# Kernel optimization log

Measured on AMD Instinct MI355X. Metric: run time of the kernel, lower is better.

## Reference

```python
import jax, jax.numpy as jnp
import numpy as np

B, T, D_IN, H, C = 4096, 20, 300, 512, 10


def setup_inputs() -> dict:
    key = jax.random.key(0)
    ks = jax.random.split(key, 12)
    s = lambda fan_in, fan_out: float(np.sqrt(6.0 / (fan_in + fan_out)))  # xavier uniform bound
    u = lambda k, shape, b: jax.random.uniform(k, shape, jnp.float32, -b, b)
    return {
        "x": jax.random.normal(ks[0], (B, T, D_IN), jnp.float32),
        "W_emb": u(ks[1], (D_IN, H), s(D_IN, H)),
        "b_emb": jnp.zeros((H,), jnp.float32),
        "wx0": u(ks[2], (H, H), s(H, H)),
        "wh0": u(ks[3], (H, H), s(H, H)),
        "b0": jnp.zeros((H,), jnp.float32),
        "wx1": u(ks[4], (H, H), s(H, H)),
        "wh1": u(ks[5], (H, H), s(H, H)),
        "b1": jnp.zeros((H,), jnp.float32),
        "wx2": u(ks[6], (H, H), s(H, H)),
        "wh2": u(ks[7], (H, H), s(H, H)),
        "b2": jnp.zeros((H,), jnp.float32),
        "W_fc": u(ks[8], (H, C), s(H, C)),
        "b_fc": jnp.zeros((C,), jnp.float32),
    }


def reference(x, W_emb, b_emb, wx0, wh0, b0, wx1, wh1, b1, wx2, wh2, b2, W_fc, b_fc):
    # embedding_layer applied to all timesteps: [B,T,300] -> [B,T,512]
    emb = jnp.einsum("btd,dh->bth", x, W_emb) + b_emb
    h0 = jnp.zeros((x.shape[0], wx0.shape[1]), x.dtype)
    init = (h0, h0, h0)

    def step(carry, v_t):  # v_t: [B,H]
        h0, h1, h2 = carry
        h0 = jnp.tanh(v_t @ wx0 + h0 @ wh0 + b0)
        h1 = jnp.tanh(h0 @ wx1 + h1 @ wh1 + b1)
        h2 = jnp.tanh(h1 @ wx2 + h2 @ wh2 + b2)
        return (h0, h1, h2), None

    (h0, h1, h2), _ = jax.lax.scan(step, init, jnp.swapaxes(emb, 0, 1))  # scan over T
    return h2 @ W_fc + b_fc  # [B, C]
```

## Files before the change

### kernel.cpp

```cpp
#include <hip/hip_runtime.h>

typedef _Float16 f16;
typedef _Float16 f16x8 __attribute__((ext_vector_type(8)));
typedef float floatx4 __attribute__((ext_vector_type(4)));

__device__ __forceinline__ float ftanh(float x) {
  float ax = __builtin_fabsf(x);
  float e  = __expf(-2.0f * ax);
  float t  = (1.0f - e) * __builtin_amdgcn_rcpf(1.0f + e);
  return x < 0.0f ? -t : t;
}

__device__ __forceinline__ void gll16(const f16* g, f16* l) {
  __builtin_amdgcn_global_load_lds(
      (const __attribute__((address_space(1))) void*)g,
      (__attribute__((address_space(3))) void*)l, 16, 0, 0);
}

template<int FJ>
__device__ __forceinline__ void tile_gemm(
    const f16* __restrict__ A0, int ldA0,
    const f16* __restrict__ A1, int ldA1,
    int K, const f16* __restrict__ WT,
    const float* __restrict__ bias,
    f16* __restrict__ outp, int bm, int bn, f16* sm)
{
  const int tid  = threadIdx.x;
  const int w    = tid >> 6;
  const int lane = tid & 63;
  const int lm   = lane & 15;
  const int quad = lane >> 4;
  const int wm   = (w >> 1) * 64;
  const int wn   = (w & 1) * (FJ * 16);
  const int srow8 = lane >> 3;
  const int scol  = ((lane & 7) ^ srow8) * 8;
  const int lmx   = lane & 7;
  constexpr int SB = 8192 + FJ * 2048;

  floatx4 acc[4][FJ];
  #pragma unroll
  for (int i = 0; i < 4; ++i)
    #pragma unroll
    for (int j = 0; j < FJ; ++j)
      acc[i][j] = (floatx4){0.f, 0.f, 0.f, 0.f};

  auto stage = [&](int buf, int k0) {
    const f16* Asrc = (k0 < 512) ? (A0 + k0) : (A1 + (k0 - 512));
    const int  ld   = (k0 < 512) ? ldA0 : ldA1;
    f16* As0 = sm + buf * SB;
    f16* Ws0 = As0 + 8192;
    #pragma unroll
    for (int i = 0; i < 4; ++i) {
      int r = (w * 4 + i) * 8 + srow8;
      gll16(Asrc + (size_t)(bm + r) * ld + scol, As0 + (w * 4 + i) * 512);
    }
    #pragma unroll
    for (int i = 0; i < FJ; ++i) {
      int r = (w * FJ + i) * 8 + srow8;
      gll16(WT + (size_t)(bn + r) * K + k0 + scol, Ws0 + (w * FJ + i) * 512);
    }
  };

  const int NS = K >> 6;
  stage(0, 0);
  __syncthreads();
  for (int s = 0; s < NS; ++s) {
    if (s + 1 < NS) stage((s + 1) & 1, (s + 1) << 6);
    const f16* As0 = sm + (s & 1) * SB;
    const f16* Ws0 = As0 + 8192;
    #pragma unroll
    for (int kk = 0; kk < 64; kk += 32) {
      const int sw = (((kk >> 3) + quad) ^ lmx) << 3;
      f16x8 a[4], bfr[FJ];
      #pragma unroll
      for (int fi = 0; fi < 4; ++fi)
        a[fi] = *(const f16x8*)&As0[(size_t)(wm + fi * 16 + lm) * 64 + sw];
      #pragma unroll
      for (int fj = 0; fj < FJ; ++fj)
        bfr[fj] = *(const f16x8*)&Ws0[(size_t)(wn + fj * 16 + lm) * 64 + sw];
      #pragma unroll
      for (int fi = 0; fi < 4; ++fi)
        #pragma unroll
        for (int fj = 0; fj < FJ; ++fj)
          acc[fi][fj] = __builtin_amdgcn_mfma_f32_16x16x32_f16(a[fi], bfr[fj], acc[fi][fj], 0, 0, 0);
    }
    __syncthreads();
  }

  constexpr int ES = FJ * 32 + 8;
  #pragma unroll
  for (int fi = 0; fi < 4; ++fi)
    #pragma unroll
    for (int fj = 0; fj < FJ; ++fj) {
      int col = wn + fj * 16 + lm;
      #pragma unroll
      for (int r = 0; r < 4; ++r) {
        int row = wm + fi * 16 + quad * 4 + r;
        sm[row * ES + col] = (f16)acc[fi][fj][r];
      }
    }
  __syncthreads();
  constexpr int TPR = (FJ * 32) / 8;
  constexpr int RPP = 256 / TPR;
  #pragma unroll
  for (int p = 0; p < 128 / RPP; ++p) {
    int row = p * RPP + tid / TPR;
    int c8  = (tid % TPR) * 8;
    f16x8 ve = *(const f16x8*)&sm[row * ES + c8];
    floatx4 bv0 = *(const floatx4*)&bias[bn + c8];
    floatx4 bv1 = *(const floatx4*)&bias[bn + c8 + 4];
    union { f16 e[8]; f16x8 v; } o;
    #pragma unroll
    for (int j = 0; j < 4; ++j) o.e[j]     = (f16)ftanh((float)ve[j]     + bv0[j]);
    #pragma unroll
    for (int j = 0; j < 4; ++j) o.e[4 + j] = (f16)ftanh((float)ve[4 + j] + bv1[j]);
    *(f16x8*)(outp + (size_t)(bm + row) * 512 + bn + c8) = o.v;
  }
}

__global__ __launch_bounds__(256, 3)
void rnn_step(int wv, const f16* __restrict__ xh,
              const f16* __restrict__ W0T, const f16* __restrict__ W1T,
              const f16* __restrict__ W2T,
              const float* __restrict__ bcomb, const float* __restrict__ b1,
              const float* __restrict__ b2,
              const f16* __restrict__ H0c, f16* __restrict__ H0n,
              const f16* __restrict__ H1c, f16* __restrict__ H1n,
              const f16* __restrict__ H2c, f16* __restrict__ H2n)
{
  __shared__ f16 sm[24576];
  const int b   = blockIdx.x;
  const int xcd = b & 7;
  const int r   = b >> 3;
  const int slab = xcd * 4 + (r & 3);
  const int bn   = ((r >> 2) & 7) * 64;

  if (r < 32) {
    if (wv > 19) return;
    tile_gemm<2>(H0c, 512, xh + (size_t)wv * 320, 6400, 832, W0T, bcomb,
                 H0n, slab * 128, bn, sm);
  } else if (r < 64) {
    if (wv < 1 || wv > 20) return;
    tile_gemm<2>(H0c, 512, H1c, 512, 1024, W1T, b1, H1n, slab * 128, bn, sm);
  } else {
    if (wv < 2) return;
    tile_gemm<2>(H1c, 512, H2c, 512, 1024, W2T, b2, H2n, slab * 128, bn, sm);
  }
}

#define PX_N 1600

__global__ __launch_bounds__(256)
void prep_x(const float* __restrict__ x, f16* __restrict__ xh)
{
  const int NTH = PX_N * 256;
  const int g = blockIdx.x * 256 + threadIdx.x;
  floatx4 va[8], vb[8];
  int rw[8], cc[8];
  const floatx4 z4 = {0.f, 0.f, 0.f, 0.f};
  #pragma unroll
  for (int s = 0; s < 8; ++s) {
    int U = g + s * NTH;
    int row = U / 40;
    int c   = (U - row * 40) * 8;
    rw[s] = row; cc[s] = c;
    const float* src = x + (size_t)row * 300 + c;
    va[s] = (c + 4 <= 300) ? *(const floatx4*)src : z4;
    vb[s] = (c + 8 <= 300) ? *(const floatx4*)(src + 4) : z4;
  }
  #pragma unroll
  for (int s = 0; s < 8; ++s) {
    union { f16 e[8]; f16x8 v; } t;
    #pragma unroll
    for (int j = 0; j < 4; ++j) { t.e[j] = (f16)va[s][j]; t.e[4 + j] = (f16)vb[s][j]; }
    *(f16x8*)(xh + (size_t)rw[s] * 320 + cc[s]) = t.v;
  }
}

#define PW_WCE 2560
#define PW_BC  2568
#define PW_WT  3208
#define PW_Z   6280

__global__ __launch_bounds__(256)
void prep_w(const float* __restrict__ W_emb, const float* __restrict__ b_emb,
            const float* __restrict__ wx0, const float* __restrict__ wh0,
            const float* __restrict__ b0,
            const float* __restrict__ wx1, const float* __restrict__ wh1,
            const float* __restrict__ wx2, const float* __restrict__ wh2,
            f16* __restrict__ W0T, f16* __restrict__ W1T, f16* __restrict__ W2T,
            float* __restrict__ bcomb,
            f16* __restrict__ H0a, f16* __restrict__ H1b, f16* __restrict__ H2a)
{
  __shared__ float red[256];
  const int b   = blockIdx.x;
  const int tid = threadIdx.x;

  if (b < PW_WCE) {
    int oidx  = b * 64 + (tid & 63);
    int chunk = tid >> 6;
    int n = oidx & 511, k = oidx >> 9;
    float s = 0.f;
    if (k < 300) {
      const float* we = W_emb + k * 512 + chunk * 128;
      const float* wx = wx0 + (size_t)(chunk * 128) * 512 + n;
      #pragma unroll 4
      for (int j = 0; j < 128; ++j)
        s = __builtin_fmaf(we[j], wx[(size_t)j * 512], s);
    }
    red[tid] = s;
    __syncthreads();
    if (chunk == 0)
      W0T[(size_t)n * 832 + 512 + k] =
          (f16)(red[tid] + red[tid + 64] + red[tid + 128] + red[tid + 192]);
  } else if (b < PW_BC) {
    int n     = (b - PW_WCE) * 64 + (tid & 63);
    int chunk = tid >> 6;
    float s = 0.f;
    const float* be = b_emb + chunk * 128;
    const float* wx = wx0 + (size_t)(chunk * 128) * 512 + n;
    #pragma unroll 4
    for (int j = 0; j < 128; ++j)
      s = __builtin_fmaf(be[j], wx[(size_t)j * 512], s);
    red[tid] = s;
    __syncthreads();
    if (chunk == 0)
      bcomb[n] = b0[n] + red[tid] + red[tid + 64] + red[tid + 128] + red[tid + 192];
  } else if (b < PW_WT) {
    int id = (b - PW_BC) * 256 + tid;
    if (id < 32768) {
      int n = id & 511, k8 = id >> 9;
      union { f16 e[8]; f16x8 v; } t;
      #pragma unroll
      for (int j = 0; j < 8; ++j) t.e[j] = (f16)wh0[(size_t)(k8 * 8 + j) * 512 + n];
      *(f16x8*)&W0T[(size_t)n * 832 + k8 * 8] = t.v;
    } else if (id < 98304) {
      int i2 = id - 32768;
      int n = i2 & 511, k8 = i2 >> 9;
      union { f16 e[8]; f16x8 v; } t;
      const float* src = (k8 < 64) ? (wx1 + (size_t)(k8 * 8) * 512 + n)
                                   : (wh1 + (size_t)((k8 - 64) * 8) * 512 + n);
      #pragma unroll
      for (int j = 0; j < 8; ++j) t.e[j] = (f16)src[(size_t)j * 512];
      *(f16x8*)&W1T[(size_t)n * 1024 + k8 * 8] = t.v;
    } else {
      int i2 = id - 98304;
      int n = i2 & 511, k8 = i2 >> 9;
      union { f16 e[8]; f16x8 v; } t;
      const float* src = (k8 < 64) ? (wx2 + (size_t)(k8 * 8) * 512 + n)
                                   : (wh2 + (size_t)((k8 - 64) * 8) * 512 + n);
      #pragma unroll
      for (int j = 0; j < 8; ++j) t.e[j] = (f16)src[(size_t)j * 512];
      *(f16x8*)&W2T[(size_t)n * 1024 + k8 * 8] = t.v;
    }
  } else {
    int id = (b - PW_WT) * 256 + tid;
    f16x8 z8 = {};
    f16* dst = (id < 262144) ? H0a : (id < 524288) ? H1b : H2a;
    *(f16x8*)(dst + (size_t)(id & 262143) * 8) = z8;
  }
}

__global__ void fc_kernel(const f16* __restrict__ h2,
                          const float* __restrict__ Wfc, const float* __restrict__ bfc,
                          float* __restrict__ out)
{
  __shared__ float wf[5120];
  __shared__ float bf[16];
  const int tid = threadIdx.x;
  for (int i = tid; i < 5120; i += 256) wf[i] = Wfc[i];
  if (tid < 10) bf[tid] = bfc[tid];
  __syncthreads();
  int id = blockIdx.x * 256 + tid;
  int row = id / 10;
  int c = id - row * 10;
  float s = bf[c];
  const f16* hr = h2 + (size_t)row * 512;
  for (int k8 = 0; k8 < 64; ++k8) {
    f16x8 h8 = *(const f16x8*)(hr + k8 * 8);
    #pragma unroll
    for (int j = 0; j < 8; ++j)
      s = __builtin_fmaf((float)h8[j], wf[(k8 * 8 + j) * 10 + c], s);
  }
  out[id] = s;
}

extern "C" void kernel_launch(void* const* d_in, const int* in_sizes, int n_in,
                              void* d_out, int out_size, void* d_ws, size_t ws_size,
                              hipStream_t stream)
{
  (void)in_sizes; (void)n_in; (void)out_size; (void)ws_size;
  const float* x     = (const float*)d_in[0];
  const float* W_emb = (const float*)d_in[1];
  const float* b_emb = (const float*)d_in[2];
  const float* wx0   = (const float*)d_in[3];
  const float* wh0   = (const float*)d_in[4];
  const float* b0    = (const float*)d_in[5];
  const float* wx1   = (const float*)d_in[6];
  const float* wh1   = (const float*)d_in[7];
  const float* b1    = (const float*)d_in[8];
  const float* wx2   = (const float*)d_in[9];
  const float* wh2   = (const float*)d_in[10];
  const float* b2    = (const float*)d_in[11];
  const float* W_fc  = (const float*)d_in[12];
  const float* b_fc  = (const float*)d_in[13];
  float* out = (float*)d_out;

  char* ws = (char*)d_ws;
  size_t off = 0;
  auto alloc = [&](size_t bytes) -> void* {
    void* p = ws + off;
    off = (off + bytes + 255) & ~(size_t)255;
    return p;
  };
  f16*   xh    = (f16*)alloc((size_t)81920 * 320 * 2);
  f16*   W0T   = (f16*)alloc((size_t)512 * 832 * 2);
  f16*   W1T   = (f16*)alloc((size_t)512 * 1024 * 2);
  f16*   W2T   = (f16*)alloc((size_t)512 * 1024 * 2);
  float* bcomb = (float*)alloc(512 * 4);
  f16*   H0a   = (f16*)alloc((size_t)4096 * 512 * 2);
  f16*   H0b   = (f16*)alloc((size_t)4096 * 512 * 2);
  f16*   H1a   = (f16*)alloc((size_t)4096 * 512 * 2);
  f16*   H1b   = (f16*)alloc((size_t)4096 * 512 * 2);
  f16*   H2a   = (f16*)alloc((size_t)4096 * 512 * 2);
  f16*   H2b   = (f16*)alloc((size_t)4096 * 512 * 2);

  prep_x<<<PX_N, 256, 0, stream>>>(x, xh);
  prep_w<<<PW_Z, 256, 0, stream>>>(W_emb, b_emb, wx0, wh0, b0,
                                   wx1, wh1, wx2, wh2,
                                   W0T, W1T, W2T, bcomb, H0a, H1b, H2a);

  for (int wv = 0; wv < 22; ++wv) {
    const int cur = wv & 1;
    f16* H0c = cur ? H0b : H0a;  f16* H0n = cur ? H0a : H0b;
    f16* H1c = cur ? H1b : H1a;  f16* H1n = cur ? H1a : H1b;
    f16* H2c = cur ? H2b : H2a;  f16* H2n = cur ? H2a : H2b;
    rnn_step<<<768, 256, 0, stream>>>(wv, xh, W0T, W1T, W2T, bcomb, b1, b2,
                                      H0c, H0n, H1c, H1n, H2c, H2n);
  }

  fc_kernel<<<160, 256, 0, stream>>>(H2a, W_fc, b_fc, out);
}
```

Measured before the change: 626.6 us.

## Widen layer-1/2 GEMM tiles, add MFMA priority, and tile W_emb·wx0 precompute in LDS

Layers 1 and 2 now use 128-column tiles (FJ=4) instead of 64, so the wavefront launch drops from 768 to 512 blocks. Shared memory grows and launch bounds fall to 2 blocks per CU to fit the larger tile. s_setprio is raised around the MFMA burst so the issuing wave gets priority. The prep_w fold of W_emb into wx0 is rewritten as an LDS-tiled 16x16 product instead of strided global reads. The larger tiles mean fewer blocks per layer-1/2 step and lower occupancy, which may hurt load balance across CUs.

```diff
diff --git a/kernel.cpp b/kernel.cpp
--- a/kernel.cpp
+++ b/kernel.cpp
@@ -78,11 +78,13 @@
       #pragma unroll
       for (int fj = 0; fj < FJ; ++fj)
         bfr[fj] = *(const f16x8*)&Ws0[(size_t)(wn + fj * 16 + lm) * 64 + sw];
+      __builtin_amdgcn_s_setprio(1);
       #pragma unroll
       for (int fi = 0; fi < 4; ++fi)
         #pragma unroll
         for (int fj = 0; fj < FJ; ++fj)
           acc[fi][fj] = __builtin_amdgcn_mfma_f32_16x16x32_f16(a[fi], bfr[fj], acc[fi][fj], 0, 0, 0);
+      __builtin_amdgcn_s_setprio(0);
     }
     __syncthreads();
   }
@@ -118,7 +120,7 @@
   }
 }
 
-__global__ __launch_bounds__(256, 3)
+__global__ __launch_bounds__(256, 2)
 void rnn_step(int wv, const f16* __restrict__ xh,
               const f16* __restrict__ W0T, const f16* __restrict__ W1T,
               const f16* __restrict__ W2T,
@@ -128,23 +130,29 @@
               const f16* __restrict__ H1c, f16* __restrict__ H1n,
               const f16* __restrict__ H2c, f16* __restrict__ H2n)
 {
-  __shared__ f16 sm[24576];
+  __shared__ f16 sm[32768];
   const int b   = blockIdx.x;
   const int xcd = b & 7;
   const int r   = b >> 3;
-  const int slab = xcd * 4 + (r & 3);
-  const int bn   = ((r >> 2) & 7) * 64;
 
   if (r < 32) {
     if (wv > 19) return;
+    const int slab = xcd * 4 + (r & 3);
+    const int bn   = (r >> 2) * 64;
     tile_gemm<2>(H0c, 512, xh + (size_t)wv * 320, 6400, 832, W0T, bcomb,
                  H0n, slab * 128, bn, sm);
-  } else if (r < 64) {
+  } else if (r < 48) {
     if (wv < 1 || wv > 20) return;
-    tile_gemm<2>(H0c, 512, H1c, 512, 1024, W1T, b1, H1n, slab * 128, bn, sm);
+    const int rr   = r - 32;
+    const int slab = xcd * 4 + (rr & 3);
+    const int bn   = (rr >> 2) * 128;
+    tile_gemm<4>(H0c, 512, H1c, 512, 1024, W1T, b1, H1n, slab * 128, bn, sm);
   } else {
     if (wv < 2) return;
-    tile_gemm<2>(H1c, 512, H2c, 512, 1024, W2T, b2, H2n, slab * 128, bn, sm);
+    const int rr   = r - 48;
+    const int slab = xcd * 4 + (rr & 3);
+    const int bn   = (rr >> 2) * 128;
+    tile_gemm<4>(H1c, 512, H2c, 512, 1024, W2T, b2, H2n, slab * 128, bn, sm);
   }
 }
 
@@ -177,10 +185,10 @@
   }
 }
 
-#define PW_WCE 2560
-#define PW_BC  2568
-#define PW_WT  3208
-#define PW_Z   6280
+#define QW_WCE 640
+#define QW_BC  648
+#define QW_WT  1288
+#define QW_Z   4360
 
 __global__ __launch_bounds__(256)
 void prep_w(const float* __restrict__ W_emb, const float* __restrict__ b_emb,
@@ -192,29 +200,39 @@
             float* __restrict__ bcomb,
             f16* __restrict__ H0a, f16* __restrict__ H1b, f16* __restrict__ H2a)
 {
-  __shared__ float red[256];
+  __shared__ float smem[16384];
   const int b   = blockIdx.x;
   const int tid = threadIdx.x;
-
-  if (b < PW_WCE) {
-    int oidx  = b * 64 + (tid & 63);
-    int chunk = tid >> 6;
-    int n = oidx & 511, k = oidx >> 9;
+  const floatx4 z4 = {0.f, 0.f, 0.f, 0.f};
+
+  if (b < QW_WCE) {
+    float* wes = smem;
+    float* wxs = smem + 8192;
+    const int kt = b >> 5, nt = b & 31;
+    const int k0 = kt * 16, n0 = nt * 16;
+    const int rr = tid >> 4, cc = tid & 15;
+    {
+      const int k = k0 + rr;
+      #pragma unroll
+      for (int q = 0; q < 8; ++q) {
+        floatx4 v = (k < 300) ? *(const floatx4*)&W_emb[(size_t)k * 512 + cc * 32 + q * 4] : z4;
+        *(floatx4*)&wes[rr * 512 + cc * 32 + q * 4] = v;
+      }
+    }
+    #pragma unroll 4
+    for (int jj = 0; jj < 32; ++jj) {
+      int j = rr * 32 + jj;
+      wxs[j * 16 + cc] = wx0[(size_t)j * 512 + n0 + cc];
+    }
+    __syncthreads();
     float s = 0.f;
-    if (k < 300) {
-      const float* we = W_emb + k * 512 + chunk * 128;
-      const float* wx = wx0 + (size_t)(chunk * 128) * 512 + n;
-      #pragma unroll 4
-      for (int j = 0; j < 128; ++j)
-        s = __builtin_fmaf(we[j], wx[(size_t)j * 512], s);
-    }
-    red[tid] = s;
-    __syncthreads();
-    if (chunk == 0)
-      W0T[(size_t)n * 832 + 512 + k] =
-          (f16)(red[tid] + red[tid + 64] + red[tid + 128] + red[tid + 192]);
-  } else if (b < PW_BC) {
-    int n     = (b - PW_WCE) * 64 + (tid & 63);
+    #pragma unroll 8
+    for (int j = 0; j < 512; ++j)
+      s = __builtin_fmaf(wes[rr * 512 + j], wxs[j * 16 + cc], s);
+    W0T[(size_t)(n0 + cc) * 832 + 512 + k0 + rr] = (f16)s;
+  } else if (b < QW_BC) {
+    float* red = smem;
+    int n     = (b - QW_WCE) * 64 + (tid & 63);
     int chunk = tid >> 6;
     float s = 0.f;
     const float* be = b_emb + chunk * 128;
@@ -226,8 +244,8 @@
     __syncthreads();
     if (chunk == 0)
       bcomb[n] = b0[n] + red[tid] + red[tid + 64] + red[tid + 128] + red[tid + 192];
-  } else if (b < PW_WT) {
-    int id = (b - PW_BC) * 256 + tid;
+  } else if (b < QW_WT) {
+    int id = (b - QW_BC) * 256 + tid;
     if (id < 32768) {
       int n = id & 511, k8 = id >> 9;
       union { f16 e[8]; f16x8 v; } t;
@@ -254,7 +272,7 @@
       *(f16x8*)&W2T[(size_t)n * 1024 + k8 * 8] = t.v;
     }
   } else {
-    int id = (b - PW_WT) * 256 + tid;
+    int id = (b - QW_WT) * 256 + tid;
     f16x8 z8 = {};
     f16* dst = (id < 262144) ? H0a : (id < 524288) ? H1b : H2a;
     *(f16x8*)(dst + (size_t)(id & 262143) * 8) = z8;
@@ -326,7 +344,7 @@
   f16*   H2b   = (f16*)alloc((size_t)4096 * 512 * 2);
 
   prep_x<<<PX_N, 256, 0, stream>>>(x, xh);
-  prep_w<<<PW_Z, 256, 0, stream>>>(W_emb, b_emb, wx0, wh0, b0,
+  prep_w<<<QW_Z, 256, 0, stream>>>(W_emb, b_emb, wx0, wh0, b0,
                                    wx1, wh1, wx2, wh2,
                                    W0T, W1T, W2T, bcomb, H0a, H1b, H2a);
 
@@ -335,7 +353,7 @@
     f16* H0c = cur ? H0b : H0a;  f16* H0n = cur ? H0a : H0b;
     f16* H1c = cur ? H1b : H1a;  f16* H1n = cur ? H1a : H1b;
     f16* H2c = cur ? H2b : H2a;  f16* H2n = cur ? H2a : H2b;
-    rnn_step<<<768, 256, 0, stream>>>(wv, xh, W0T, W1T, W2T, bcomb, b1, b2,
+    rnn_step<<<512, 256, 0, stream>>>(wv, xh, W0T, W1T, W2T, bcomb, b1, b2,
                                       H0c, H0n, H1c, H1n, H2c, H2n);
   }
 
```

Result: faster. 553.0 us (-11.7%).
